# Kernel optimization log

Hardware: AMD Instinct MI355X
Metric: run time of the kernel (lower is better)

## Reference

```python
import jax, jax.numpy as jnp
import numpy as np

EMB = 768
HEADS = 12
HEAD_DIM = EMB // HEADS
SEQ = 4096
BATCH = 1


def setup_inputs() -> dict:
    key = jax.random.key(0)
    ks = jax.random.split(key, 9)
    s = 1.0 / np.sqrt(EMB)
    return {
        "x": jax.random.normal(ks[0], (BATCH, SEQ, EMB), dtype=jnp.float32),
        "wq": jax.random.normal(ks[1], (EMB, EMB), dtype=jnp.float32) * s,
        "bq": jax.random.normal(ks[2], (EMB,), dtype=jnp.float32) * s,
        "wk": jax.random.normal(ks[3], (EMB, EMB), dtype=jnp.float32) * s,
        "bk": jax.random.normal(ks[4], (EMB,), dtype=jnp.float32) * s,
        "wv": jax.random.normal(ks[5], (EMB, EMB), dtype=jnp.float32) * s,
        "bv": jax.random.normal(ks[6], (EMB,), dtype=jnp.float32) * s,
        "wo": jax.random.normal(ks[7], (EMB, EMB), dtype=jnp.float32) * s,
        "bo": jax.random.normal(ks[8], (EMB,), dtype=jnp.float32) * s,
    }


def reference(x, wq, bq, wk, bk, wv, bv, wo, bo):
    b, n, _ = x.shape
    # projections: [b, n, emb] -> [b, heads, n, head_dim]
    def split_heads(t):
        return t.reshape(b, n, HEADS, HEAD_DIM).transpose(0, 2, 1, 3)
    q = split_heads(x @ wq + bq)
    k = split_heads(x @ wk + bk)
    v = split_heads(x @ wv + bv)
    # full N x N scores (naive attention, as in the original)
    scores = jnp.einsum("bhqd,bhkd->bhqk", q, k)
    causal = jnp.triu(jnp.ones((n, n), dtype=bool), k=1)
    scores = jnp.where(causal, -jnp.inf, scores)
    weights = jax.nn.softmax(scores / np.sqrt(HEAD_DIM), axis=-1)
    # dropout with rate 0.0 is identity (eval mode)
    ctx = jnp.einsum("bhqk,bhkd->bhqd", weights, v)
    ctx = ctx.transpose(0, 2, 1, 3).reshape(b, n, EMB)
    return ctx @ wo + bo
```

## Files before the change

kernel.cpp:

```cpp
#include <hip/hip_runtime.h>
#include <stdint.h>

#define SEQ 4096
#define EMB 768
#define HEADS 12
#define HD 64
#define NQT (SEQ / 64)

typedef __attribute__((ext_vector_type(8))) short short8;
typedef __attribute__((ext_vector_type(4))) short short4v;
typedef __attribute__((ext_vector_type(8))) __bf16 bf16x8;
typedef __attribute__((ext_vector_type(4))) __bf16 bf16x4;
typedef __attribute__((ext_vector_type(4))) float f32x4;

#define QSCALE 0.18033688011112043f

static __device__ __forceinline__ unsigned short f2bf(float f) {
    unsigned int u = __builtin_bit_cast(unsigned int, f);
    unsigned int r = 0x7fffu + ((u >> 16) & 1u);
    u += r;
    return (unsigned short)(u >> 16);
}

static __device__ __forceinline__ f32x4 mfma32(short8 a, short8 b, f32x4 c) {
    return __builtin_amdgcn_mfma_f32_16x16x32_bf16(
        __builtin_bit_cast(bf16x8, a), __builtin_bit_cast(bf16x8, b), c, 0, 0, 0);
}

static __device__ __forceinline__ f32x4 mfma16(short4v a, short4v b, f32x4 c) {
#if __has_builtin(__builtin_amdgcn_mfma_f32_16x16x16_bf16)
    return __builtin_amdgcn_mfma_f32_16x16x16_bf16(
        __builtin_bit_cast(bf16x4, a), __builtin_bit_cast(bf16x4, b), c, 0, 0, 0);
#else
    return __builtin_amdgcn_mfma_f32_16x16x16bf16_1k(a, b, c, 0, 0, 0);
#endif
}

static __device__ __forceinline__ short4v pack4bf(float a, float b, float c, float d) {
#if __has_builtin(__builtin_amdgcn_cvt_pk_bf16_f32)
    typedef __attribute__((ext_vector_type(2))) __bf16 bf16x2;
    bf16x2 lo = __builtin_amdgcn_cvt_pk_bf16_f32(a, b);
    bf16x2 hi = __builtin_amdgcn_cvt_pk_bf16_f32(c, d);
    uint2 u = {__builtin_bit_cast(unsigned int, lo), __builtin_bit_cast(unsigned int, hi)};
    return __builtin_bit_cast(short4v, u);
#else
    short4v p;
    p[0] = (short)f2bf(a); p[1] = (short)f2bf(b);
    p[2] = (short)f2bf(c); p[3] = (short)f2bf(d);
    return p;
#endif
}

static __device__ __forceinline__ void load_lds16(const void* g, void* l) {
    __builtin_amdgcn_global_load_lds(
        (const __attribute__((address_space(1))) unsigned int*)(uintptr_t)g,
        (__attribute__((address_space(3))) unsigned int*)(uintptr_t)l, 16, 0, 0);
}

static __device__ __forceinline__ int pid_of(int h, int qt, int ch) {
    int b = (qt < 40) ? (qt - 20) : (qt < 60 ? 20 + (qt - 40) * 2 : 60 + (qt - 60) * 3);
    return h * 72 + b + (ch - 1);
}

__global__ __launch_bounds__(256) void convert_all(const float* __restrict__ x,
                                                   const float* __restrict__ wq,
                                                   const float* __restrict__ wk,
                                                   const float* __restrict__ wv,
                                                   const float* __restrict__ wo,
                                                   unsigned short* __restrict__ xb,
                                                   unsigned short* __restrict__ wqkvT,
                                                   unsigned short* __restrict__ woT) {
    __shared__ float Ls[64][65];
    const int bid = blockIdx.x;
    if (bid < 3072) {
        int i = bid * 256 + threadIdx.x;
        float4 v = ((const float4*)x)[i];
        ushort4 o = {f2bf(v.x), f2bf(v.y), f2bf(v.z), f2bf(v.w)};
        ((ushort4*)xb)[i] = o;
        return;
    }
    const int idx = bid - 3072;
    const int z = idx / 144;
    const int bx = (idx % 144) / 12, by = idx % 12;
    const float* W = (z == 0) ? wq : (z == 1) ? wk : (z == 2) ? wv : wo;
    unsigned short* dst = (z < 3) ? (wqkvT + (size_t)z * EMB * EMB) : woT;
    const int k0 = bx * 64, n0 = by * 64;
    const int r = threadIdx.x >> 2, c0 = (threadIdx.x & 3) * 16;
    for (int j = 0; j < 16; j += 4) {
        float4 v = *(const float4*)&W[(size_t)(k0 + r) * EMB + n0 + c0 + j];
        Ls[r][c0 + j] = v.x;
        Ls[r][c0 + j + 1] = v.y;
        Ls[r][c0 + j + 2] = v.z;
        Ls[r][c0 + j + 3] = v.w;
    }
    __syncthreads();
    unsigned short tmp[16];
    for (int j = 0; j < 16; j++) tmp[j] = f2bf(Ls[c0 + j][r]);
    *(uint4*)&dst[(size_t)(n0 + r) * EMB + k0 + c0] = *(uint4*)tmp;
    *(uint4*)&dst[(size_t)(n0 + r) * EMB + k0 + c0 + 8] = *(uint4*)(tmp + 8);
}

__global__ __launch_bounds__(256) void gemm_qkv(const unsigned short* __restrict__ A,
                                                const unsigned short* __restrict__ Bt,
                                                const float* __restrict__ b0p,
                                                const float* __restrict__ b1p,
                                                const float* __restrict__ b2p,
                                                unsigned short* __restrict__ QKb,
                                                unsigned short* __restrict__ Vtb) {
    __shared__ __align__(16) unsigned short SMEM[8192];
    unsigned short* As = SMEM;
    unsigned short* Bs = SMEM + 4096;
    const int tid = threadIdx.x;
    const int wave = tid >> 6, lane = tid & 63, quad = lane >> 4, l16 = lane & 15;
    const int m0 = blockIdx.x * 128, n0 = blockIdx.y * 128;
    const int wm = (wave >> 1) * 64, wn = (wave & 1) * 64;
    const int lrow = lane >> 2, lcol = (lane & 3) * 8;

    f32x4 acc[4][4] = {};

    for (int k0 = 0; k0 < EMB; k0 += 32) {
        __syncthreads();
        for (int t = 0; t < 2; t++) {
            int row = wave * 32 + t * 16 + lrow;
            load_lds16(&A[(size_t)(m0 + row) * EMB + k0 + lcol], &As[(wave * 2 + t) * 512]);
            load_lds16(&Bt[(size_t)(n0 + row) * EMB + k0 + lcol], &Bs[(wave * 2 + t) * 512]);
        }
        __syncthreads();
        short8 a[4], b[4];
        for (int i = 0; i < 4; i++) a[i] = *(const short8*)&As[(wm + i * 16 + l16) * 32 + quad * 8];
        for (int i = 0; i < 4; i++) b[i] = *(const short8*)&Bs[(wn + i * 16 + l16) * 32 + quad * 8];
        for (int i = 0; i < 4; i++)
            for (int j = 0; j < 4; j++) acc[i][j] = mfma32(a[i], b[j], acc[i][j]);
    }

    const int z = n0 / EMB;
    if (z < 2) {
        const float* bias = z ? b1p : b0p;
        const float sc = z ? 1.0f : QSCALE;
        for (int i = 0; i < 4; i++)
            for (int j = 0; j < 4; j++) {
                int mbase = m0 + wm + i * 16 + quad * 4;
                int n = n0 + wn + j * 16 + l16;
                float bv = bias[n - z * EMB];
                for (int r = 0; r < 4; r++)
                    QKb[(size_t)(mbase + r) * 1536 + n] = f2bf((acc[i][j][r] + bv) * sc);
            }
    } else {
        const int nn = n0 + wn + l16 - 2 * EMB;
        for (int j = 0; j < 4; j++) {
            __syncthreads();
            const float bv = b2p[nn + j * 16];
            const int nloc = (wave & 1) * 16 + l16;
            for (int i = 0; i < 4; i++) {
                ushort4 pk;
                pk.x = f2bf(acc[i][j][0] + bv);
                pk.y = f2bf(acc[i][j][1] + bv);
                pk.z = f2bf(acc[i][j][2] + bv);
                pk.w = f2bf(acc[i][j][3] + bv);
                *(ushort4*)&SMEM[nloc * 136 + wm + i * 16 + quad * 4] = pk;
            }
            __syncthreads();
            const int nl = tid >> 3, c = tid & 7;
            const int ng = (nl >> 4) * 64 + j * 16 + (nl & 15) + n0 + 0 * 0 - 2 * EMB;
            const int hh = ng >> 6, dd = ng & 63;
            unsigned short* dst = &Vtb[(size_t)(hh * HD + dd) * SEQ + m0];
            *(uint4*)&dst[c * 8] = *(uint4*)&SMEM[nl * 136 + c * 8];
            *(uint4*)&dst[64 + c * 8] = *(uint4*)&SMEM[nl * 136 + 64 + c * 8];
        }
    }
}

__global__ __launch_bounds__(256) void gemm_out(const unsigned short* __restrict__ A,
                                                const unsigned short* __restrict__ Bt,
                                                const float* __restrict__ bias,
                                                float* __restrict__ outp) {
    __shared__ __align__(16) unsigned short As[64 * 32];
    __shared__ __align__(16) unsigned short Bs[128 * 32];
    const int tid = threadIdx.x;
    const int wave = tid >> 6, lane = tid & 63, quad = lane >> 4, l16 = lane & 15;
    const int m0 = blockIdx.x * 64, n0 = blockIdx.y * 128;
    const int wm = (wave >> 1) * 32, wn = (wave & 1) * 64;
    const int lrow = lane >> 2, lcol = (lane & 3) * 8;

    f32x4 acc[2][4] = {};

    for (int k0 = 0; k0 < EMB; k0 += 32) {
        __syncthreads();
        load_lds16(&A[(size_t)(m0 + wave * 16 + lrow) * EMB + k0 + lcol], &As[wave * 512]);
        for (int t = 0; t < 2; t++) {
            int row = wave * 32 + t * 16 + lrow;
            load_lds16(&Bt[(size_t)(n0 + row) * EMB + k0 + lcol], &Bs[(wave * 2 + t) * 512]);
        }
        __syncthreads();
        short8 a[2], b[4];
        for (int i = 0; i < 2; i++) a[i] = *(const short8*)&As[(wm + i * 16 + l16) * 32 + quad * 8];
        for (int j = 0; j < 4; j++) b[j] = *(const short8*)&Bs[(wn + j * 16 + l16) * 32 + quad * 8];
        for (int i = 0; i < 2; i++)
            for (int j = 0; j < 4; j++) acc[i][j] = mfma32(a[i], b[j], acc[i][j]);
    }

    for (int i = 0; i < 2; i++)
        for (int j = 0; j < 4; j++) {
            int mbase = m0 + wm + i * 16 + quad * 4;
            int n = n0 + wn + j * 16 + l16;
            float bv = bias[n];
            for (int r = 0; r < 4; r++) outp[(size_t)(mbase + r) * EMB + n] = acc[i][j][r] + bv;
        }
}

__global__ __launch_bounds__(256) void attn_kernel(const unsigned short* __restrict__ QKb,
                                                   const unsigned short* __restrict__ Vtb,
                                                   unsigned short* __restrict__ ctxb,
                                                   unsigned short* __restrict__ Op,
                                                   float* __restrict__ mArr,
                                                   float* __restrict__ lArr) {
    __shared__ __align__(16) unsigned short Ks[64 * 64];
    __shared__ __align__(16) unsigned short Vs[64 * 64];

    const int bid = blockIdx.x;
    const int h = bid % HEADS;
    const int rem = 135 - bid / HEADS;
    int qt, ch, nch;
    if (rem < 20) {
        qt = rem; ch = 0; nch = 1;
    } else if (rem < 60) {
        int t = rem - 20; qt = 20 + (t >> 1); ch = t & 1; nch = 2;
    } else if (rem < 120) {
        int t = rem - 60; qt = 40 + t / 3; ch = t % 3; nch = 3;
    } else {
        int t = rem - 120; qt = 60 + (t >> 2); ch = t & 3; nch = 4;
    }
    const int kb = ch * (qt + 1) / nch;
    const int ke = (ch + 1) * (qt + 1) / nch - 1;
    const int qbase = qt * 64;
    const int tid = threadIdx.x;
    const int wave = tid >> 6, lane = tid & 63, quad = lane >> 4, l16 = lane & 15;

    const unsigned short* Qg = QKb + (size_t)h * HD;
    const unsigned short* Kg = QKb + (size_t)(EMB + h * HD);
    const unsigned short* Vh = Vtb + (size_t)h * HD * SEQ;

    const int q = qbase + wave * 16 + l16;
    const short8 bQ0 = *(const short8*)&Qg[(size_t)q * 1536 + quad * 8];
    const short8 bQ1 = *(const short8*)&Qg[(size_t)q * 1536 + 32 + quad * 8];

    const int row = tid >> 2, t4 = tid & 3, cg = t4 * 16;
    const int swk = row & 7, swv = row & 15;

    f32x4 O[4] = {};
    float m_i = -3.0e38f, l_i = 0.f;

    uint4 kr0, kr1, vr0, vr1;
    {
        const int kb64 = kb * 64;
        kr0 = *(const uint4*)&Kg[(size_t)(kb64 + row) * 1536 + cg];
        kr1 = *(const uint4*)&Kg[(size_t)(kb64 + row) * 1536 + cg + 8];
        vr0 = *(const uint4*)&Vh[(size_t)row * SEQ + kb64 + cg];
        vr1 = *(const uint4*)&Vh[(size_t)row * SEQ + kb64 + cg + 8];
    }

    for (int kt = kb; kt <= ke; kt++) {
        const int kbase = kt * 64;
        __syncthreads();
        *(uint4*)&Ks[row * 64 + ((2 * t4) ^ swk) * 8] = kr0;
        *(uint4*)&Ks[row * 64 + ((2 * t4 + 1) ^ swk) * 8] = kr1;
        *(uint2*)&Vs[row * 64 + ((4 * t4) ^ swv) * 4] = ((const uint2*)&vr0)[0];
        *(uint2*)&Vs[row * 64 + ((4 * t4 + 1) ^ swv) * 4] = ((const uint2*)&vr0)[1];
        *(uint2*)&Vs[row * 64 + ((4 * t4 + 2) ^ swv) * 4] = ((const uint2*)&vr1)[0];
        *(uint2*)&Vs[row * 64 + ((4 * t4 + 3) ^ swv) * 4] = ((const uint2*)&vr1)[1];
        if (kt < ke) {
            const int nb = kbase + 64;
            kr0 = *(const uint4*)&Kg[(size_t)(nb + row) * 1536 + cg];
            kr1 = *(const uint4*)&Kg[(size_t)(nb + row) * 1536 + cg + 8];
            vr0 = *(const uint4*)&Vh[(size_t)row * SEQ + nb + cg];
            vr1 = *(const uint4*)&Vh[(size_t)row * SEQ + nb + cg + 8];
        }
        __syncthreads();

        const int swr = l16 & 7;
        f32x4 st[4];
        for (int nt = 0; nt < 4; nt++) {
            short8 aK0 = *(const short8*)&Ks[(nt * 16 + l16) * 64 + (quad ^ swr) * 8];
            short8 aK1 = *(const short8*)&Ks[(nt * 16 + l16) * 64 + ((quad + 4) ^ swr) * 8];
            f32x4 z = {};
            z = mfma32(aK0, bQ0, z);
            z = mfma32(aK1, bQ1, z);
            st[nt] = z;
        }
        if (kt == qt) {
            for (int nt = 0; nt < 4; nt++)
                for (int r = 0; r < 4; r++)
                    if (kbase + nt * 16 + quad * 4 + r > q) st[nt][r] = -INFINITY;
        }
        float mx = -3.0e38f;
        for (int nt = 0; nt < 4; nt++)
            for (int r = 0; r < 4; r++) mx = fmaxf(mx, st[nt][r]);
        mx = fmaxf(mx, __shfl_xor(mx, 16));
        mx = fmaxf(mx, __shfl_xor(mx, 32));
        const bool inc = mx > m_i;
        if (__ballot(inc)) {
            const float mn = inc ? mx : m_i;
            const float alpha = __builtin_amdgcn_exp2f(m_i - mn);
            m_i = mn;
            l_i *= alpha;
            for (int dt = 0; dt < 4; dt++)
                for (int r = 0; r < 4; r++) O[dt][r] *= alpha;
        }
        float rs = 0.f;
        short4v pk[4];
        for (int nt = 0; nt < 4; nt++) {
            float p0 = __builtin_amdgcn_exp2f(st[nt][0] - m_i);
            float p1 = __builtin_amdgcn_exp2f(st[nt][1] - m_i);
            float p2 = __builtin_amdgcn_exp2f(st[nt][2] - m_i);
            float p3 = __builtin_amdgcn_exp2f(st[nt][3] - m_i);
            rs += p0 + p1 + p2 + p3;
            pk[nt] = pack4bf(p0, p1, p2, p3);
        }
        rs += __shfl_xor(rs, 16);
        rs += __shfl_xor(rs, 32);
        l_i += rs;
        for (int dt = 0; dt < 4; dt++)
            for (int nt = 0; nt < 4; nt++) {
                short4v av = *(const short4v*)&Vs[(dt * 16 + l16) * 64 + ((4 * nt + quad) ^ l16) * 4];
                O[dt] = mfma16(av, pk[nt], O[dt]);
            }
    }

    const int ql = wave * 16 + l16;
    if (nch == 1) {
        const float inv = 1.f / l_i;
        for (int dt = 0; dt < 4; dt++) {
            ushort4 o;
            o.x = f2bf(O[dt][0] * inv);
            o.y = f2bf(O[dt][1] * inv);
            o.z = f2bf(O[dt][2] * inv);
            o.w = f2bf(O[dt][3] * inv);
            *(ushort4*)&ctxb[(size_t)q * EMB + h * HD + dt * 16 + quad * 4] = o;
        }
    } else {
        if (ch == 0) {
            for (int dt = 0; dt < 4; dt++) {
                ushort4 o;
                o.x = f2bf(O[dt][0]);
                o.y = f2bf(O[dt][1]);
                o.z = f2bf(O[dt][2]);
                o.w = f2bf(O[dt][3]);
                *(ushort4*)&ctxb[(size_t)q * EMB + h * HD + dt * 16 + quad * 4] = o;
            }
        } else {
            const int pid = pid_of(h, qt, ch);
            for (int dt = 0; dt < 4; dt++) {
                ushort4 o;
                o.x = f2bf(O[dt][0]);
                o.y = f2bf(O[dt][1]);
                o.z = f2bf(O[dt][2]);
                o.w = f2bf(O[dt][3]);
                *(ushort4*)&Op[(size_t)pid * 4096 + ql * 64 + dt * 16 + quad * 4] = o;
            }
        }
        if (quad == 0) {
            const int mli = ((h * 64 + qt) * 4 + ch) * 64 + ql;
            mArr[mli] = m_i;
            lArr[mli] = l_i;
        }
    }
}

__global__ __launch_bounds__(256) void merge_kernel(const unsigned short* __restrict__ Op,
                                                    const float* __restrict__ mArr,
                                                    const float* __restrict__ lArr,
                                                    unsigned short* __restrict__ ctxb) {
    const int gid = blockIdx.x;
    const int h = gid / 44;
    const int qt = 20 + gid % 44;
    const int nch = (qt < 40) ? 2 : (qt < 60) ? 3 : 4;
    const int q = threadIdx.x >> 2, d0 = (threadIdx.x & 3) * 16;
    const int mlbase = (h * 64 + qt) * 4;

    float mc[4], lc[4];
    for (int c = 0; c < nch; c++) {
        mc[c] = mArr[(mlbase + c) * 64 + q];
        lc[c] = lArr[(mlbase + c) * 64 + q];
    }
    float M = mc[0];
    for (int c = 1; c < nch; c++) M = fmaxf(M, mc[c]);
    float w[4], L = 0.f;
    for (int c = 0; c < nch; c++) {
        w[c] = __builtin_amdgcn_exp2f(mc[c] - M);
        L += w[c] * lc[c];
    }
    const float inv = 1.f / L;
    for (int c = 0; c < nch; c++) w[c] *= inv;

    unsigned short* dst = &ctxb[(size_t)(qt * 64 + q) * EMB + h * HD + d0];
    for (int jj = 0; jj < 16; jj += 8) {
        uint4 u0 = *(const uint4*)&dst[jj];
        float f[8];
        const unsigned short* p0 = (const unsigned short*)&u0;
        for (int t = 0; t < 8; t++)
            f[t] = w[0] * __builtin_bit_cast(float, (unsigned int)p0[t] << 16);
        for (int c = 1; c < nch; c++) {
            const int pid = pid_of(h, qt, c);
            uint4 u = *(const uint4*)&Op[(size_t)pid * 4096 + q * 64 + d0 + jj];
            const unsigned short* p = (const unsigned short*)&u;
            for (int t = 0; t < 8; t++)
                f[t] += w[c] * __builtin_bit_cast(float, (unsigned int)p[t] << 16);
        }
        unsigned short o[8];
        for (int t = 0; t < 8; t++) o[t] = f2bf(f[t]);
        *(uint4*)&dst[jj] = *(uint4*)o;
    }
}

extern "C" void kernel_launch(void* const* d_in, const int* in_sizes, int n_in,
                              void* d_out, int out_size, void* d_ws, size_t ws_size,
                              hipStream_t stream) {
    const float* x = (const float*)d_in[0];
    const float* wq = (const float*)d_in[1];
    const float* bq = (const float*)d_in[2];
    const float* wk = (const float*)d_in[3];
    const float* bk = (const float*)d_in[4];
    const float* wv = (const float*)d_in[5];
    const float* bv = (const float*)d_in[6];
    const float* wo = (const float*)d_in[7];
    const float* bo = (const float*)d_in[8];

    unsigned short* ws = (unsigned short*)d_ws;
    unsigned short* xb = ws;
    unsigned short* wqkvT = xb + SEQ * EMB;
    unsigned short* woT = wqkvT + 3 * EMB * EMB;
    unsigned short* QKb = woT + EMB * EMB;
    unsigned short* Vtb = QKb + (size_t)SEQ * 1536;
    unsigned short* ctxb = Vtb + HEADS * SEQ * HD;
    unsigned short* Op = xb;
    float* mArr = (float*)(ws + 864 * 4096);
    float* lArr = mArr + 12 * 64 * 4 * 64;

    convert_all<<<dim3(3072 + 576), 256, 0, stream>>>(x, wq, wk, wv, wo, xb, wqkvT, woT);
    gemm_qkv<<<dim3(SEQ / 128, 3 * EMB / 128), 256, 0, stream>>>(
        xb, wqkvT, bq, bk, bv, QKb, Vtb);
    attn_kernel<<<dim3(12 * 136), 256, 0, stream>>>(QKb, Vtb, ctxb, Op, mArr, lArr);
    merge_kernel<<<dim3(528), 256, 0, stream>>>(Op, mArr, lArr, ctxb);
    gemm_out<<<dim3(SEQ / 64, EMB / 128), 256, 0, stream>>>(ctxb, woT, bo, (float*)d_out);
}
```

Before: 205.3 us.

## Use 128-row query tiles in attention and unroll GEMM K-loops to 64

The attention kernel moves from 64-query blocks of 256 threads to 128-query blocks of 512 threads. Each K/V tile loaded into LDS is now shared by twice as many query rows, and waves whose rows lie entirely before a key tile skip it, which reworks the split-K chunking and merge indexing. Both GEMMs now stage two 32-wide K slices per barrier pair, halving the number of synchronisations at the cost of more LDS. The softmax update is factored into a helper function. The larger blocks mean fewer resident workgroups and more intra-block idle waves near the causal diagonal.

```diff
diff --git a/kernel.cpp b/kernel.cpp
--- a/kernel.cpp
+++ b/kernel.cpp
@@ -5,7 +5,6 @@
 #define EMB 768
 #define HEADS 12
 #define HD 64
-#define NQT (SEQ / 64)
 
 typedef __attribute__((ext_vector_type(8))) short short8;
 typedef __attribute__((ext_vector_type(4))) short short4v;
@@ -57,9 +56,40 @@
         (__attribute__((address_space(3))) unsigned int*)(uintptr_t)l, 16, 0, 0);
 }
 
-static __device__ __forceinline__ int pid_of(int h, int qt, int ch) {
-    int b = (qt < 40) ? (qt - 20) : (qt < 60 ? 20 + (qt - 40) * 2 : 60 + (qt - 60) * 3);
-    return h * 72 + b + (ch - 1);
+static __device__ __forceinline__ int pid_of(int h, int i128, int ch) {
+    int b = (i128 < 20) ? (i128 - 10)
+                        : (i128 < 30 ? 10 + (i128 - 20) * 2 : 30 + (i128 - 30) * 3);
+    return h * 36 + b + (ch - 1);
+}
+
+static __device__ __forceinline__ void softmax_step(f32x4* st, float& m_i, float& l_i,
+                                                    f32x4* O, short4v* pk) {
+    float mx = -3.0e38f;
+    for (int nt = 0; nt < 4; nt++)
+        for (int r = 0; r < 4; r++) mx = fmaxf(mx, st[nt][r]);
+    mx = fmaxf(mx, __shfl_xor(mx, 16));
+    mx = fmaxf(mx, __shfl_xor(mx, 32));
+    const bool inc = mx > m_i;
+    if (__ballot(inc)) {
+        const float mn = inc ? mx : m_i;
+        const float alpha = __builtin_amdgcn_exp2f(m_i - mn);
+        m_i = mn;
+        l_i *= alpha;
+        for (int dt = 0; dt < 4; dt++)
+            for (int r = 0; r < 4; r++) O[dt][r] *= alpha;
+    }
+    float rs = 0.f;
+    for (int nt = 0; nt < 4; nt++) {
+        float p0 = __builtin_amdgcn_exp2f(st[nt][0] - m_i);
+        float p1 = __builtin_amdgcn_exp2f(st[nt][1] - m_i);
+        float p2 = __builtin_amdgcn_exp2f(st[nt][2] - m_i);
+        float p3 = __builtin_amdgcn_exp2f(st[nt][3] - m_i);
+        rs += p0 + p1 + p2 + p3;
+        pk[nt] = pack4bf(p0, p1, p2, p3);
+    }
+    rs += __shfl_xor(rs, 16);
+    rs += __shfl_xor(rs, 32);
+    l_i += rs;
 }
 
 __global__ __launch_bounds__(256) void convert_all(const float* __restrict__ x,
@@ -107,9 +137,11 @@
                                                 const float* __restrict__ b2p,
                                                 unsigned short* __restrict__ QKb,
                                                 unsigned short* __restrict__ Vtb) {
-    __shared__ __align__(16) unsigned short SMEM[8192];
-    unsigned short* As = SMEM;
-    unsigned short* Bs = SMEM + 4096;
+    __shared__ __align__(16) unsigned short SMEM[16384];
+    unsigned short* As0 = SMEM;
+    unsigned short* Bs0 = SMEM + 4096;
+    unsigned short* As1 = SMEM + 8192;
+    unsigned short* Bs1 = SMEM + 12288;
     const int tid = threadIdx.x;
     const int wave = tid >> 6, lane = tid & 63, quad = lane >> 4, l16 = lane & 15;
     const int m0 = blockIdx.x * 128, n0 = blockIdx.y * 128;
@@ -118,19 +150,34 @@
 
     f32x4 acc[4][4] = {};
 
-    for (int k0 = 0; k0 < EMB; k0 += 32) {
+    for (int k0 = 0; k0 < EMB; k0 += 64) {
         __syncthreads();
         for (int t = 0; t < 2; t++) {
             int row = wave * 32 + t * 16 + lrow;
-            load_lds16(&A[(size_t)(m0 + row) * EMB + k0 + lcol], &As[(wave * 2 + t) * 512]);
-            load_lds16(&Bt[(size_t)(n0 + row) * EMB + k0 + lcol], &Bs[(wave * 2 + t) * 512]);
-        }
-        __syncthreads();
-        short8 a[4], b[4];
-        for (int i = 0; i < 4; i++) a[i] = *(const short8*)&As[(wm + i * 16 + l16) * 32 + quad * 8];
-        for (int i = 0; i < 4; i++) b[i] = *(const short8*)&Bs[(wn + i * 16 + l16) * 32 + quad * 8];
-        for (int i = 0; i < 4; i++)
-            for (int j = 0; j < 4; j++) acc[i][j] = mfma32(a[i], b[j], acc[i][j]);
+            load_lds16(&A[(size_t)(m0 + row) * EMB + k0 + lcol], &As0[(wave * 2 + t) * 512]);
+            load_lds16(&Bt[(size_t)(n0 + row) * EMB + k0 + lcol], &Bs0[(wave * 2 + t) * 512]);
+            load_lds16(&A[(size_t)(m0 + row) * EMB + k0 + 32 + lcol], &As1[(wave * 2 + t) * 512]);
+            load_lds16(&Bt[(size_t)(n0 + row) * EMB + k0 + 32 + lcol], &Bs1[(wave * 2 + t) * 512]);
+        }
+        __syncthreads();
+        {
+            short8 a[4], b[4];
+            for (int i = 0; i < 4; i++)
+                a[i] = *(const short8*)&As0[(wm + i * 16 + l16) * 32 + quad * 8];
+            for (int i = 0; i < 4; i++)
+                b[i] = *(const short8*)&Bs0[(wn + i * 16 + l16) * 32 + quad * 8];
+            for (int i = 0; i < 4; i++)
+                for (int j = 0; j < 4; j++) acc[i][j] = mfma32(a[i], b[j], acc[i][j]);
+        }
+        {
+            short8 a[4], b[4];
+            for (int i = 0; i < 4; i++)
+                a[i] = *(const short8*)&As1[(wm + i * 16 + l16) * 32 + quad * 8];
+            for (int i = 0; i < 4; i++)
+                b[i] = *(const short8*)&Bs1[(wn + i * 16 + l16) * 32 + quad * 8];
+            for (int i = 0; i < 4; i++)
+                for (int j = 0; j < 4; j++) acc[i][j] = mfma32(a[i], b[j], acc[i][j]);
+        }
     }
 
     const int z = n0 / EMB;
@@ -161,7 +208,7 @@
             }
             __syncthreads();
             const int nl = tid >> 3, c = tid & 7;
-            const int ng = (nl >> 4) * 64 + j * 16 + (nl & 15) + n0 + 0 * 0 - 2 * EMB;
+            const int ng = (nl >> 4) * 64 + j * 16 + (nl & 15) + n0 - 2 * EMB;
             const int hh = ng >> 6, dd = ng & 63;
             unsigned short* dst = &Vtb[(size_t)(hh * HD + dd) * SEQ + m0];
             *(uint4*)&dst[c * 8] = *(uint4*)&SMEM[nl * 136 + c * 8];
@@ -174,8 +221,11 @@
                                                 const unsigned short* __restrict__ Bt,
                                                 const float* __restrict__ bias,
                                                 float* __restrict__ outp) {
-    __shared__ __align__(16) unsigned short As[64 * 32];
-    __shared__ __align__(16) unsigned short Bs[128 * 32];
+    __shared__ __align__(16) unsigned short SMEM[12288];
+    unsigned short* As0 = SMEM;
+    unsigned short* As1 = SMEM + 2048;
+    unsigned short* Bs0 = SMEM + 4096;
+    unsigned short* Bs1 = SMEM + 8192;
     const int tid = threadIdx.x;
     const int wave = tid >> 6, lane = tid & 63, quad = lane >> 4, l16 = lane & 15;
     const int m0 = blockIdx.x * 64, n0 = blockIdx.y * 128;
@@ -184,19 +234,34 @@
 
     f32x4 acc[2][4] = {};
 
-    for (int k0 = 0; k0 < EMB; k0 += 32) {
-        __syncthreads();
-        load_lds16(&A[(size_t)(m0 + wave * 16 + lrow) * EMB + k0 + lcol], &As[wave * 512]);
+    for (int k0 = 0; k0 < EMB; k0 += 64) {
+        __syncthreads();
+        load_lds16(&A[(size_t)(m0 + wave * 16 + lrow) * EMB + k0 + lcol], &As0[wave * 512]);
+        load_lds16(&A[(size_t)(m0 + wave * 16 + lrow) * EMB + k0 + 32 + lcol], &As1[wave * 512]);
         for (int t = 0; t < 2; t++) {
             int row = wave * 32 + t * 16 + lrow;
-            load_lds16(&Bt[(size_t)(n0 + row) * EMB + k0 + lcol], &Bs[(wave * 2 + t) * 512]);
-        }
-        __syncthreads();
-        short8 a[2], b[4];
-        for (int i = 0; i < 2; i++) a[i] = *(const short8*)&As[(wm + i * 16 + l16) * 32 + quad * 8];
-        for (int j = 0; j < 4; j++) b[j] = *(const short8*)&Bs[(wn + j * 16 + l16) * 32 + quad * 8];
-        for (int i = 0; i < 2; i++)
-            for (int j = 0; j < 4; j++) acc[i][j] = mfma32(a[i], b[j], acc[i][j]);
+            load_lds16(&Bt[(size_t)(n0 + row) * EMB + k0 + lcol], &Bs0[(wave * 2 + t) * 512]);
+            load_lds16(&Bt[(size_t)(n0 + row) * EMB + k0 + 32 + lcol], &Bs1[(wave * 2 + t) * 512]);
+        }
+        __syncthreads();
+        {
+            short8 a[2], b[4];
+            for (int i = 0; i < 2; i++)
+                a[i] = *(const short8*)&As0[(wm + i * 16 + l16) * 32 + quad * 8];
+            for (int j = 0; j < 4; j++)
+                b[j] = *(const short8*)&Bs0[(wn + j * 16 + l16) * 32 + quad * 8];
+            for (int i = 0; i < 2; i++)
+                for (int j = 0; j < 4; j++) acc[i][j] = mfma32(a[i], b[j], acc[i][j]);
+        }
+        {
+            short8 a[2], b[4];
+            for (int i = 0; i < 2; i++)
+                a[i] = *(const short8*)&As1[(wm + i * 16 + l16) * 32 + quad * 8];
+            for (int j = 0; j < 4; j++)
+                b[j] = *(const short8*)&Bs1[(wn + j * 16 + l16) * 32 + quad * 8];
+            for (int i = 0; i < 2; i++)
+                for (int j = 0; j < 4; j++) acc[i][j] = mfma32(a[i], b[j], acc[i][j]);
+        }
     }
 
     for (int i = 0; i < 2; i++)
@@ -208,7 +273,7 @@
         }
 }
 
-__global__ __launch_bounds__(256) void attn_kernel(const unsigned short* __restrict__ QKb,
+__global__ __launch_bounds__(512) void attn_kernel(const unsigned short* __restrict__ QKb,
                                                    const unsigned short* __restrict__ Vtb,
                                                    unsigned short* __restrict__ ctxb,
                                                    unsigned short* __restrict__ Op,
@@ -219,20 +284,21 @@
 
     const int bid = blockIdx.x;
     const int h = bid % HEADS;
-    const int rem = 135 - bid / HEADS;
-    int qt, ch, nch;
-    if (rem < 20) {
-        qt = rem; ch = 0; nch = 1;
-    } else if (rem < 60) {
-        int t = rem - 20; qt = 20 + (t >> 1); ch = t & 1; nch = 2;
-    } else if (rem < 120) {
-        int t = rem - 60; qt = 40 + t / 3; ch = t % 3; nch = 3;
+    const int r2 = 67 - bid / HEADS;
+    int i128, ch, nch;
+    if (r2 < 10) {
+        i128 = r2; ch = 0; nch = 1;
+    } else if (r2 < 30) {
+        int t = r2 - 10; i128 = 10 + (t >> 1); ch = t & 1; nch = 2;
+    } else if (r2 < 60) {
+        int t = r2 - 30; i128 = 20 + t / 3; ch = t % 3; nch = 3;
     } else {
-        int t = rem - 120; qt = 60 + (t >> 2); ch = t & 3; nch = 4;
-    }
-    const int kb = ch * (qt + 1) / nch;
-    const int ke = (ch + 1) * (qt + 1) / nch - 1;
-    const int qbase = qt * 64;
+        int t = r2 - 60; i128 = 30 + (t >> 2); ch = t & 3; nch = 4;
+    }
+    const int T = 2 * i128 + 2;
+    const int kb = ch * T / nch;
+    const int ke = (ch + 1) * T / nch - 1;
+    const int qbase = i128 * 128;
     const int tid = threadIdx.x;
     const int wave = tid >> 6, lane = tid & 63, quad = lane >> 4, l16 = lane & 15;
 
@@ -244,38 +310,33 @@
     const short8 bQ0 = *(const short8*)&Qg[(size_t)q * 1536 + quad * 8];
     const short8 bQ1 = *(const short8*)&Qg[(size_t)q * 1536 + 32 + quad * 8];
 
-    const int row = tid >> 2, t4 = tid & 3, cg = t4 * 16;
+    const int row = tid >> 3, t8 = tid & 7;
     const int swk = row & 7, swv = row & 15;
 
     f32x4 O[4] = {};
     float m_i = -3.0e38f, l_i = 0.f;
 
-    uint4 kr0, kr1, vr0, vr1;
+    uint4 kr, vr;
     {
         const int kb64 = kb * 64;
-        kr0 = *(const uint4*)&Kg[(size_t)(kb64 + row) * 1536 + cg];
-        kr1 = *(const uint4*)&Kg[(size_t)(kb64 + row) * 1536 + cg + 8];
-        vr0 = *(const uint4*)&Vh[(size_t)row * SEQ + kb64 + cg];
-        vr1 = *(const uint4*)&Vh[(size_t)row * SEQ + kb64 + cg + 8];
+        kr = *(const uint4*)&Kg[(size_t)(kb64 + row) * 1536 + t8 * 8];
+        vr = *(const uint4*)&Vh[(size_t)row * SEQ + kb64 + t8 * 8];
     }
 
     for (int kt = kb; kt <= ke; kt++) {
         const int kbase = kt * 64;
         __syncthreads();
-        *(uint4*)&Ks[row * 64 + ((2 * t4) ^ swk) * 8] = kr0;
-        *(uint4*)&Ks[row * 64 + ((2 * t4 + 1) ^ swk) * 8] = kr1;
-        *(uint2*)&Vs[row * 64 + ((4 * t4) ^ swv) * 4] = ((const uint2*)&vr0)[0];
-        *(uint2*)&Vs[row * 64 + ((4 * t4 + 1) ^ swv) * 4] = ((const uint2*)&vr0)[1];
-        *(uint2*)&Vs[row * 64 + ((4 * t4 + 2) ^ swv) * 4] = ((const uint2*)&vr1)[0];
-        *(uint2*)&Vs[row * 64 + ((4 * t4 + 3) ^ swv) * 4] = ((const uint2*)&vr1)[1];
+        *(uint4*)&Ks[row * 64 + (t8 ^ swk) * 8] = kr;
+        *(uint2*)&Vs[row * 64 + ((2 * t8) ^ swv) * 4] = ((const uint2*)&vr)[0];
+        *(uint2*)&Vs[row * 64 + ((2 * t8 + 1) ^ swv) * 4] = ((const uint2*)&vr)[1];
         if (kt < ke) {
             const int nb = kbase + 64;
-            kr0 = *(const uint4*)&Kg[(size_t)(nb + row) * 1536 + cg];
-            kr1 = *(const uint4*)&Kg[(size_t)(nb + row) * 1536 + cg + 8];
-            vr0 = *(const uint4*)&Vh[(size_t)row * SEQ + nb + cg];
-            vr1 = *(const uint4*)&Vh[(size_t)row * SEQ + nb + cg + 8];
-        }
-        __syncthreads();
+            kr = *(const uint4*)&Kg[(size_t)(nb + row) * 1536 + t8 * 8];
+            vr = *(const uint4*)&Vh[(size_t)row * SEQ + nb + t8 * 8];
+        }
+        __syncthreads();
+
+        if (kbase > qbase + wave * 16 + 15) continue;
 
         const int swr = l16 & 7;
         f32x4 st[4];
@@ -287,41 +348,19 @@
             z = mfma32(aK1, bQ1, z);
             st[nt] = z;
         }
-        if (kt == qt) {
+        if (kbase + 63 > qbase + wave * 16) {
             for (int nt = 0; nt < 4; nt++)
                 for (int r = 0; r < 4; r++)
                     if (kbase + nt * 16 + quad * 4 + r > q) st[nt][r] = -INFINITY;
         }
-        float mx = -3.0e38f;
-        for (int nt = 0; nt < 4; nt++)
-            for (int r = 0; r < 4; r++) mx = fmaxf(mx, st[nt][r]);
-        mx = fmaxf(mx, __shfl_xor(mx, 16));
-        mx = fmaxf(mx, __shfl_xor(mx, 32));
-        const bool inc = mx > m_i;
-        if (__ballot(inc)) {
-            const float mn = inc ? mx : m_i;
-            const float alpha = __builtin_amdgcn_exp2f(m_i - mn);
-            m_i = mn;
-            l_i *= alpha;
-            for (int dt = 0; dt < 4; dt++)
-                for (int r = 0; r < 4; r++) O[dt][r] *= alpha;
-        }
-        float rs = 0.f;
+
         short4v pk[4];
-        for (int nt = 0; nt < 4; nt++) {
-            float p0 = __builtin_amdgcn_exp2f(st[nt][0] - m_i);
-            float p1 = __builtin_amdgcn_exp2f(st[nt][1] - m_i);
-            float p2 = __builtin_amdgcn_exp2f(st[nt][2] - m_i);
-            float p3 = __builtin_amdgcn_exp2f(st[nt][3] - m_i);
-            rs += p0 + p1 + p2 + p3;
-            pk[nt] = pack4bf(p0, p1, p2, p3);
-        }
-        rs += __shfl_xor(rs, 16);
-        rs += __shfl_xor(rs, 32);
-        l_i += rs;
+        softmax_step(st, m_i, l_i, O, pk);
+
         for (int dt = 0; dt < 4; dt++)
             for (int nt = 0; nt < 4; nt++) {
-                short4v av = *(const short4v*)&Vs[(dt * 16 + l16) * 64 + ((4 * nt + quad) ^ l16) * 4];
+                short4v av =
+                    *(const short4v*)&Vs[(dt * 16 + l16) * 64 + ((4 * nt + quad) ^ l16) * 4];
                 O[dt] = mfma16(av, pk[nt], O[dt]);
             }
     }
@@ -348,18 +387,18 @@
                 *(ushort4*)&ctxb[(size_t)q * EMB + h * HD + dt * 16 + quad * 4] = o;
             }
         } else {
-            const int pid = pid_of(h, qt, ch);
+            const int pid = pid_of(h, i128, ch);
             for (int dt = 0; dt < 4; dt++) {
                 ushort4 o;
                 o.x = f2bf(O[dt][0]);
                 o.y = f2bf(O[dt][1]);
                 o.z = f2bf(O[dt][2]);
                 o.w = f2bf(O[dt][3]);
-                *(ushort4*)&Op[(size_t)pid * 4096 + ql * 64 + dt * 16 + quad * 4] = o;
+                *(ushort4*)&Op[(size_t)pid * 8192 + ql * 64 + dt * 16 + quad * 4] = o;
             }
         }
         if (quad == 0) {
-            const int mli = ((h * 64 + qt) * 4 + ch) * 64 + ql;
+            const int mli = ((h * 32 + i128) * 4 + ch) * 128 + ql;
             mArr[mli] = m_i;
             lArr[mli] = l_i;
         }
@@ -371,16 +410,16 @@
                                                     const float* __restrict__ lArr,
                                                     unsigned short* __restrict__ ctxb) {
     const int gid = blockIdx.x;
-    const int h = gid / 44;
-    const int qt = 20 + gid % 44;
-    const int nch = (qt < 40) ? 2 : (qt < 60) ? 3 : 4;
-    const int q = threadIdx.x >> 2, d0 = (threadIdx.x & 3) * 16;
-    const int mlbase = (h * 64 + qt) * 4;
+    const int h = gid % HEADS;
+    const int i128 = 10 + gid / HEADS;
+    const int nch = (i128 < 20) ? 2 : (i128 < 30) ? 3 : 4;
+    const int q = threadIdx.x >> 1, d0 = (threadIdx.x & 1) * 32;
+    const int mlbase = (h * 32 + i128) * 4;
 
     float mc[4], lc[4];
     for (int c = 0; c < nch; c++) {
-        mc[c] = mArr[(mlbase + c) * 64 + q];
-        lc[c] = lArr[(mlbase + c) * 64 + q];
+        mc[c] = mArr[(mlbase + c) * 128 + q];
+        lc[c] = lArr[(mlbase + c) * 128 + q];
     }
     float M = mc[0];
     for (int c = 1; c < nch; c++) M = fmaxf(M, mc[c]);
@@ -392,16 +431,16 @@
     const float inv = 1.f / L;
     for (int c = 0; c < nch; c++) w[c] *= inv;
 
-    unsigned short* dst = &ctxb[(size_t)(qt * 64 + q) * EMB + h * HD + d0];
-    for (int jj = 0; jj < 16; jj += 8) {
+    unsigned short* dst = &ctxb[(size_t)(i128 * 128 + q) * EMB + h * HD + d0];
+    for (int jj = 0; jj < 32; jj += 8) {
         uint4 u0 = *(const uint4*)&dst[jj];
         float f[8];
         const unsigned short* p0 = (const unsigned short*)&u0;
         for (int t = 0; t < 8; t++)
             f[t] = w[0] * __builtin_bit_cast(float, (unsigned int)p0[t] << 16);
         for (int c = 1; c < nch; c++) {
-            const int pid = pid_of(h, qt, c);
-            uint4 u = *(const uint4*)&Op[(size_t)pid * 4096 + q * 64 + d0 + jj];
+            const int pid = pid_of(h, i128, c);
+            uint4 u = *(const uint4*)&Op[(size_t)pid * 8192 + q * 64 + d0 + jj];
             const unsigned short* p = (const unsigned short*)&u;
             for (int t = 0; t < 8; t++)
                 f[t] += w[c] * __builtin_bit_cast(float, (unsigned int)p[t] << 16);
@@ -433,13 +472,13 @@
     unsigned short* Vtb = QKb + (size_t)SEQ * 1536;
     unsigned short* ctxb = Vtb + HEADS * SEQ * HD;
     unsigned short* Op = xb;
-    float* mArr = (float*)(ws + 864 * 4096);
-    float* lArr = mArr + 12 * 64 * 4 * 64;
+    float* mArr = (float*)(ws + 3538944);
+    float* lArr = mArr + 196608;
 
     convert_all<<<dim3(3072 + 576), 256, 0, stream>>>(x, wq, wk, wv, wo, xb, wqkvT, woT);
     gemm_qkv<<<dim3(SEQ / 128, 3 * EMB / 128), 256, 0, stream>>>(
         xb, wqkvT, bq, bk, bv, QKb, Vtb);
-    attn_kernel<<<dim3(12 * 136), 256, 0, stream>>>(QKb, Vtb, ctxb, Op, mArr, lArr);
-    merge_kernel<<<dim3(528), 256, 0, stream>>>(Op, mArr, lArr, ctxb);
+    attn_kernel<<<dim3(12 * 68), 512, 0, stream>>>(QKb, Vtb, ctxb, Op, mArr, lArr);
+    merge_kernel<<<dim3(264), 256, 0, stream>>>(Op, mArr, lArr, ctxb);
     gemm_out<<<dim3(SEQ / 64, EMB / 128), 256, 0, stream>>>(ctxb, woT, bo, (float*)d_out);
 }
```

Result: faster. 193.2 us (-5.9%).
